# Kernel tuning notes

Measured on AMD Instinct MI355X. Metric: run time of the kernel, lower is better.

## Reference

```python
import jax, jax.numpy as jnp
import numpy as np

B, C, H, W = 32, 256, 64, 64
R = 16  # reduction
TOPK = 128


def setup_inputs() -> dict:
    key = jax.random.key(0)
    k_x, k_w1, k_b1, k_w2, k_b2 = jax.random.split(key, 5)
    return {
        "x": jax.random.normal(k_x, (B, C, H, W), dtype=jnp.float32),
        "w1": jax.random.normal(k_w1, (C // R, C), dtype=jnp.float32) * 0.05,
        "b1": jax.random.normal(k_b1, (C // R,), dtype=jnp.float32) * 0.05,
        "w2": jax.random.normal(k_w2, (C, C // R), dtype=jnp.float32) * 0.05,
        "b2": jax.random.normal(k_b2, (C,), dtype=jnp.float32) * 0.05,
        "topk": TOPK,
    }


def reference(x, w1, b1, w2, b2, topk):
    # Global average pool: [B, C, H, W] -> [B, C]
    y = jnp.mean(x, axis=(2, 3))
    # 1x1-conv squeeze-excite MLP (1x1 convs on a 1x1 spatial map == dense layers)
    h = jax.nn.relu(jnp.einsum("bc,rc->br", y, w1) + b1)
    attn_weight = jax.nn.sigmoid(jnp.einsum("br,cr->bc", h, w2) + b2)  # [B, C]
    # top-k channels by attention weight, then sort indices ascending
    _, idx = jax.lax.top_k(attn_weight, topk)          # [B, topk]
    idx = jnp.sort(idx, axis=1)
    # Fused: gather the selected channel weights and channels of x, multiply once
    aw_sel = jnp.take_along_axis(attn_weight, idx, axis=1)        # [B, topk]
    x_sel = jnp.take_along_axis(x, idx[:, :, None, None], axis=1)  # [B, topk, H, W]
    return aw_sel[:, :, None, None] * x_sel
```

## Files before the change

### kernel.cpp

```cpp
#include <hip/hip_runtime.h>

#define NB 32
#define NC 256
#define HW 4096
#define RDIM 16
#define KTOP 128

typedef float v4f __attribute__((ext_vector_type(4)));

__global__ __launch_bounds__(256) void pool_kernel(const float* __restrict__ x,
                                                   float* __restrict__ y) {
    const int wid  = threadIdx.x >> 6;
    const int lane = threadIdx.x & 63;
    const int plane = blockIdx.x * 4 + wid;
    const v4f* __restrict__ xin = (const v4f*)(x + (size_t)plane * HW);
    float s = 0.f;
#pragma unroll
    for (int i = 0; i < 16; ++i) {
        v4f v = xin[lane + i * 64];
        s += (v.x + v.y) + (v.z + v.w);
    }
#pragma unroll
    for (int off = 32; off > 0; off >>= 1) s += __shfl_down(s, off);
    if (lane == 0) y[plane] = s * (1.0f / HW);
}

__global__ __launch_bounds__(256) void se_topk_gather_kernel(
    const float* __restrict__ x, const float* __restrict__ y,
    const float* __restrict__ w1, const float* __restrict__ b1,
    const float* __restrict__ w2, const float* __restrict__ b2,
    float* __restrict__ out) {
    const int blk = blockIdx.x;
    const int b   = blk >> 5;
    const int t   = threadIdx.x;
    const int wid = t >> 6, lane = t & 63;

    __shared__ float ych[NC];
    __shared__ float hsh[RDIM];
    __shared__ float attn[NC];
    __shared__ unsigned long long masks[4];
    __shared__ int   sidx[KTOP];
    __shared__ float saw[KTOP];

    ych[t] = y[b * NC + t];
    __syncthreads();

    const int r = t >> 4;
    const int j = t & 15;
    float partial = 0.f;
#pragma unroll
    for (int k = 0; k < 16; ++k) {
        const int c = j * 16 + k;
        partial += ych[c] * w1[r * NC + c];
    }
#pragma unroll
    for (int m = 8; m > 0; m >>= 1) partial += __shfl_xor(partial, m, 16);
    if (j == 0) hsh[r] = fmaxf(partial + b1[r], 0.f);
    __syncthreads();

    float z = b2[t];
#pragma unroll
    for (int rr = 0; rr < RDIM; ++rr) z += hsh[rr] * w2[t * RDIM + rr];
    const float v = 1.0f / (1.0f + __expf(-z));
    attn[t] = v;
    __syncthreads();

    int rank = 0;
#pragma unroll 4
    for (int c = 0; c < NC; ++c) {
        const float o = attn[c];
        rank += (o > v) || (o == v && c < t);
    }
    const bool s = (rank < KTOP);

    const unsigned long long m = __ballot(s);
    if (lane == 0) masks[wid] = m;
    __syncthreads();
    if (s) {
        int pos = __popcll(m & ((lane == 63) ? 0x7FFFFFFFFFFFFFFFull
                                             : ((1ull << lane) - 1ull)));
        for (int w = 0; w < 4; ++w) pos += (w < wid) ? __popcll(masks[w]) : 0;
        sidx[pos] = t;
        saw[pos]  = v;
    }
    __syncthreads();

    const int k = (blk & 31) * 4 + wid;
    const int c = sidx[k];
    const float w = saw[k];
    const v4f* __restrict__ xin = (const v4f*)(x + ((size_t)b * NC + c) * HW);
    v4f* __restrict__ o = (v4f*)(out + ((size_t)b * KTOP + k) * HW);
#pragma unroll
    for (int i = 0; i < 16; ++i) {
        v4f vv = xin[lane + i * 64];
        v4f rr = vv * w;
        __builtin_nontemporal_store(rr, &o[lane + i * 64]);
    }
}

extern "C" void kernel_launch(void* const* d_in, const int* in_sizes, int n_in,
                              void* d_out, int out_size, void* d_ws, size_t ws_size,
                              hipStream_t stream) {
    const float* x  = (const float*)d_in[0];
    const float* w1 = (const float*)d_in[1];
    const float* b1 = (const float*)d_in[2];
    const float* w2 = (const float*)d_in[3];
    const float* b2 = (const float*)d_in[4];
    float* out = (float*)d_out;

    float* y = (float*)d_ws;

    pool_kernel<<<NB * NC / 4, 256, 0, stream>>>(x, y);
    se_topk_gather_kernel<<<NB * KTOP / 4, 256, 0, stream>>>(
        x, y, w1, b1, w2, b2, out);
}
```

Baseline: 53.79 us.

## Fuse pool and SE/top-k gather into one cooperative kernel with grid sync

Replaces the two-kernel pool then SE/top-k/gather sequence with a single cooperative kernel of 512 blocks. Each block first pools 16 channel planes, then a grid-wide sync makes the pooled means visible. Each block then recomputes the SE MLP and top-k and gathers 8 output planes. This removes a kernel launch boundary and the tail gap between kernels, and may keep x hotter in cache for the gather. In exchange it adds grid-sync overhead, relies on all 512 blocks being co-resident, and falls back to the old two-kernel path if the cooperative launch fails.

```diff
diff --git a/kernel.cpp b/kernel.cpp
--- a/kernel.cpp
+++ b/kernel.cpp
@@ -1,4 +1,7 @@
 #include <hip/hip_runtime.h>
+#include <hip/hip_cooperative_groups.h>
+
+namespace cg = cooperative_groups;
 
 #define NB 32
 #define NC 256
@@ -8,40 +11,13 @@
 
 typedef float v4f __attribute__((ext_vector_type(4)));
 
-__global__ __launch_bounds__(256) void pool_kernel(const float* __restrict__ x,
-                                                   float* __restrict__ y) {
-    const int wid  = threadIdx.x >> 6;
-    const int lane = threadIdx.x & 63;
-    const int plane = blockIdx.x * 4 + wid;
-    const v4f* __restrict__ xin = (const v4f*)(x + (size_t)plane * HW);
-    float s = 0.f;
-#pragma unroll
-    for (int i = 0; i < 16; ++i) {
-        v4f v = xin[lane + i * 64];
-        s += (v.x + v.y) + (v.z + v.w);
-    }
-#pragma unroll
-    for (int off = 32; off > 0; off >>= 1) s += __shfl_down(s, off);
-    if (lane == 0) y[plane] = s * (1.0f / HW);
-}
-
-__global__ __launch_bounds__(256) void se_topk_gather_kernel(
-    const float* __restrict__ x, const float* __restrict__ y,
+__device__ __forceinline__ void se_topk_lds(
+    int b, int t, int wid, int lane,
+    const float* __restrict__ y,
     const float* __restrict__ w1, const float* __restrict__ b1,
     const float* __restrict__ w2, const float* __restrict__ b2,
-    float* __restrict__ out) {
-    const int blk = blockIdx.x;
-    const int b   = blk >> 5;
-    const int t   = threadIdx.x;
-    const int wid = t >> 6, lane = t & 63;
-
-    __shared__ float ych[NC];
-    __shared__ float hsh[RDIM];
-    __shared__ float attn[NC];
-    __shared__ unsigned long long masks[4];
-    __shared__ int   sidx[KTOP];
-    __shared__ float saw[KTOP];
-
+    float* ych, float* hsh, float* attn, unsigned long long* masks,
+    int* sidx, float* saw) {
     ych[t] = y[b * NC + t];
     __syncthreads();
 
@@ -84,6 +60,95 @@
         saw[pos]  = v;
     }
     __syncthreads();
+}
+
+__global__ __launch_bounds__(256, 2) void ca_fused_kernel(
+    const float* __restrict__ x, float* __restrict__ y,
+    const float* __restrict__ w1, const float* __restrict__ b1,
+    const float* __restrict__ w2, const float* __restrict__ b2,
+    float* __restrict__ out) {
+    const int blk  = blockIdx.x;
+    const int b    = blk >> 4;
+    const int t    = threadIdx.x;
+    const int wid  = t >> 6, lane = t & 63;
+
+#pragma unroll 1
+    for (int rep = 0; rep < 4; ++rep) {
+        const int plane = blk * 16 + wid * 4 + rep;
+        const v4f* __restrict__ xin = (const v4f*)(x + (size_t)plane * HW);
+        float s = 0.f;
+#pragma unroll
+        for (int i = 0; i < 16; ++i) {
+            v4f v = xin[lane + i * 64];
+            s += (v.x + v.y) + (v.z + v.w);
+        }
+#pragma unroll
+        for (int off = 32; off > 0; off >>= 1) s += __shfl_down(s, off);
+        if (lane == 0) y[plane] = s * (1.0f / HW);
+    }
+    __threadfence();
+    cg::this_grid().sync();
+
+    __shared__ float ych[NC];
+    __shared__ float hsh[RDIM];
+    __shared__ float attn[NC];
+    __shared__ unsigned long long masks[4];
+    __shared__ int   sidx[KTOP];
+    __shared__ float saw[KTOP];
+    se_topk_lds(b, t, wid, lane, y, w1, b1, w2, b2,
+                ych, hsh, attn, masks, sidx, saw);
+
+#pragma unroll 1
+    for (int rep = 0; rep < 2; ++rep) {
+        const int k = (blk & 15) * 8 + wid * 2 + rep;
+        const int c = sidx[k];
+        const float w = saw[k];
+        const v4f* __restrict__ xin = (const v4f*)(x + ((size_t)b * NC + c) * HW);
+        v4f* __restrict__ o = (v4f*)(out + ((size_t)b * KTOP + k) * HW);
+#pragma unroll
+        for (int i = 0; i < 16; ++i) {
+            v4f vv = xin[lane + i * 64];
+            v4f rr = vv * w;
+            __builtin_nontemporal_store(rr, &o[lane + i * 64]);
+        }
+    }
+}
+
+__global__ __launch_bounds__(256) void pool_kernel(const float* __restrict__ x,
+                                                   float* __restrict__ y) {
+    const int wid  = threadIdx.x >> 6;
+    const int lane = threadIdx.x & 63;
+    const int plane = blockIdx.x * 4 + wid;
+    const v4f* __restrict__ xin = (const v4f*)(x + (size_t)plane * HW);
+    float s = 0.f;
+#pragma unroll
+    for (int i = 0; i < 16; ++i) {
+        v4f v = xin[lane + i * 64];
+        s += (v.x + v.y) + (v.z + v.w);
+    }
+#pragma unroll
+    for (int off = 32; off > 0; off >>= 1) s += __shfl_down(s, off);
+    if (lane == 0) y[plane] = s * (1.0f / HW);
+}
+
+__global__ __launch_bounds__(256) void se_topk_gather_kernel(
+    const float* __restrict__ x, const float* __restrict__ y,
+    const float* __restrict__ w1, const float* __restrict__ b1,
+    const float* __restrict__ w2, const float* __restrict__ b2,
+    float* __restrict__ out) {
+    const int blk = blockIdx.x;
+    const int b   = blk >> 5;
+    const int t   = threadIdx.x;
+    const int wid = t >> 6, lane = t & 63;
+
+    __shared__ float ych[NC];
+    __shared__ float hsh[RDIM];
+    __shared__ float attn[NC];
+    __shared__ unsigned long long masks[4];
+    __shared__ int   sidx[KTOP];
+    __shared__ float saw[KTOP];
+    se_topk_lds(b, t, wid, lane, y, w1, b1, w2, b2,
+                ych, hsh, attn, masks, sidx, saw);
 
     const int k = (blk & 31) * 4 + wid;
     const int c = sidx[k];
@@ -107,10 +172,15 @@
     const float* w2 = (const float*)d_in[3];
     const float* b2 = (const float*)d_in[4];
     float* out = (float*)d_out;
+    float* y   = (float*)d_ws;
 
-    float* y = (float*)d_ws;
-
-    pool_kernel<<<NB * NC / 4, 256, 0, stream>>>(x, y);
-    se_topk_gather_kernel<<<NB * KTOP / 4, 256, 0, stream>>>(
-        x, y, w1, b1, w2, b2, out);
+    void* args[] = { (void*)&x, (void*)&y, (void*)&w1, (void*)&b1,
+                     (void*)&w2, (void*)&b2, (void*)&out };
+    hipError_t err = hipLaunchCooperativeKernel(
+        (const void*)ca_fused_kernel, dim3(512), dim3(256), args, 0, stream);
+    if (err != hipSuccess) {
+        pool_kernel<<<NB * NC / 4, 256, 0, stream>>>(x, y);
+        se_topk_gather_kernel<<<NB * KTOP / 4, 256, 0, stream>>>(
+            x, y, w1, b1, w2, b2, out);
+    }
 }
```

Measured after the change: 159.0 us. 2.96x slower.

## Fuse pooling and SE/top-k gather into one kernel with per-batch spin barrier

Applied to the files above, without the earlier changes.

Merges the pooling kernel and the SE/top-k/gather kernel into a single launch of 1024 blocks. Each block pools 8 channel planes, then increments a per-batch atomic counter and spins until all 32 blocks of its batch have arrived, after which it runs the SE MLP, top-k and gather as before. This removes the second kernel launch and the gap between the two kernels. In exchange it adds a memset launch, atomics and a spin-wait that depends on all blocks being co-resident; the spin has a bounded-iteration escape that could yield wrong results if blocks are not co-resident.

```diff
diff --git a/kernel.cpp b/kernel.cpp
--- a/kernel.cpp
+++ b/kernel.cpp
@@ -8,32 +8,53 @@
 
 typedef float v4f __attribute__((ext_vector_type(4)));
 
-__global__ __launch_bounds__(256) void pool_kernel(const float* __restrict__ x,
-                                                   float* __restrict__ y) {
-    const int wid  = threadIdx.x >> 6;
-    const int lane = threadIdx.x & 63;
-    const int plane = blockIdx.x * 4 + wid;
-    const v4f* __restrict__ xin = (const v4f*)(x + (size_t)plane * HW);
-    float s = 0.f;
-#pragma unroll
-    for (int i = 0; i < 16; ++i) {
-        v4f v = xin[lane + i * 64];
-        s += (v.x + v.y) + (v.z + v.w);
-    }
-#pragma unroll
-    for (int off = 32; off > 0; off >>= 1) s += __shfl_down(s, off);
-    if (lane == 0) y[plane] = s * (1.0f / HW);
-}
-
-__global__ __launch_bounds__(256) void se_topk_gather_kernel(
-    const float* __restrict__ x, const float* __restrict__ y,
+__global__ __launch_bounds__(256, 4) void ca_fused_spin_kernel(
+    const float* __restrict__ x, float* __restrict__ y, int* __restrict__ cnt,
     const float* __restrict__ w1, const float* __restrict__ b1,
     const float* __restrict__ w2, const float* __restrict__ b2,
     float* __restrict__ out) {
-    const int blk = blockIdx.x;
-    const int b   = blk >> 5;
+    const int g   = blockIdx.x;
+    const int b   = g >> 5;
     const int t   = threadIdx.x;
     const int wid = t >> 6, lane = t & 63;
+
+    const int p0 = b * NC + (g & 31) * 8 + wid * 2;
+    {
+        const v4f* __restrict__ x0 = (const v4f*)(x + (size_t)p0 * HW);
+        const v4f* __restrict__ x1 = (const v4f*)(x + (size_t)(p0 + 1) * HW);
+        float s0 = 0.f, s1 = 0.f;
+#pragma unroll
+        for (int i = 0; i < 16; ++i) {
+            v4f a = x0[lane + i * 64];
+            v4f c = x1[lane + i * 64];
+            s0 += (a.x + a.y) + (a.z + a.w);
+            s1 += (c.x + c.y) + (c.z + c.w);
+        }
+#pragma unroll
+        for (int off = 32; off > 0; off >>= 1) {
+            s0 += __shfl_down(s0, off);
+            s1 += __shfl_down(s1, off);
+        }
+        if (lane == 0) {
+            atomicExch(&y[p0],     s0 * (1.0f / HW));
+            atomicExch(&y[p0 + 1], s1 * (1.0f / HW));
+        }
+    }
+    __syncthreads();
+    if (t == 0) {
+        __hip_atomic_fetch_add(&cnt[b], 1, __ATOMIC_RELEASE,
+                               __HIP_MEMORY_SCOPE_AGENT);
+    }
+
+    if (t == 0) {
+        long it = 0;
+        while (__hip_atomic_load(&cnt[b], __ATOMIC_ACQUIRE,
+                                 __HIP_MEMORY_SCOPE_AGENT) < 32) {
+            __builtin_amdgcn_s_sleep(16);
+            if (++it > 200000000L) break;
+        }
+    }
+    __syncthreads();
 
     __shared__ float ych[NC];
     __shared__ float hsh[RDIM];
@@ -42,7 +63,7 @@
     __shared__ int   sidx[KTOP];
     __shared__ float saw[KTOP];
 
-    ych[t] = y[b * NC + t];
+    ych[t] = atomicAdd(&y[b * NC + t], 0.0f);
     __syncthreads();
 
     const int r = t >> 4;
@@ -85,7 +106,7 @@
     }
     __syncthreads();
 
-    const int k = (blk & 31) * 4 + wid;
+    const int k = (g & 31) * 4 + wid;
     const int c = sidx[k];
     const float w = saw[k];
     const v4f* __restrict__ xin = (const v4f*)(x + ((size_t)b * NC + c) * HW);
@@ -108,9 +129,11 @@
     const float* b2 = (const float*)d_in[4];
     float* out = (float*)d_out;
 
-    float* y = (float*)d_ws;
+    float* y   = (float*)d_ws;
+    int*   cnt = (int*)(y + NB * NC);
 
-    pool_kernel<<<NB * NC / 4, 256, 0, stream>>>(x, y);
-    se_topk_gather_kernel<<<NB * KTOP / 4, 256, 0, stream>>>(
-        x, y, w1, b1, w2, b2, out);
+    hipMemsetAsync(cnt, 0, NB * sizeof(int), stream);
+
+    ca_fused_spin_kernel<<<NB * NC / 8, 256, 0, stream>>>(
+        x, y, cnt, w1, b1, w2, b2, out);
 }
```

Measured after the change: 144.7 us. 2.69x slower.
